# Kernel tuning notes

Measured on AMD Instinct MI355X. Metric: run time of the kernel, lower is better.

## Reference

```python
import jax, jax.numpy as jnp
import numpy as np

B, D, H, W = 2, 32, 192, 192
N_SIGMA = 3
K = 8  # max instance id; ids are 1..K, 0 = background
FG_W = 1.0
W_INST, W_VAR, W_SEED = 1.0, 10.0, 1.0


def _make_xyzm():
    # channel 0 = x (varies along W), 1 = y (along H), 2 = z (along D); pixel_{x,y,z}=1
    xm = jnp.broadcast_to(jnp.linspace(0.0, 1.0, W).reshape(1, 1, W), (D, H, W))
    ym = jnp.broadcast_to(jnp.linspace(0.0, 1.0, H).reshape(1, H, 1), (D, H, W))
    zm = jnp.broadcast_to(jnp.linspace(0.0, 1.0, D).reshape(D, 1, 1), (D, H, W))
    return jnp.stack([xm, ym, zm], 0)  # (3, D, H, W)


def setup_inputs() -> dict:
    key = jax.random.key(0)
    k1, k2, k3, k4 = jax.random.split(key, 4)
    prediction = jax.random.normal(k1, (B, 3 + N_SIGMA + 1, D, H, W), jnp.float32)
    instances = jax.random.randint(k2, (B, D, H, W), 0, K + 1, jnp.int32)
    labels = jax.random.randint(k3, (B, D, H, W), 0, 2, jnp.int32)
    center_images = jax.random.uniform(k4, (B, D, H, W)) < 5e-4  # sparse center flags
    return {"prediction": prediction, "xyzm": _make_xyzm(),
            "instances": instances, "labels": labels, "center_images": center_images}


def _lovasz_hinge_flat(logits, labels):
    # logits, labels: (N,) flat; labels in {0,1} float
    signs = 2.0 * labels - 1.0
    errors = 1.0 - logits * signs
    order = jnp.argsort(-errors)          # descending errors
    errors_s = errors[order]
    gt_s = labels[order]
    gts = gt_s.sum()
    inter = gts - jnp.cumsum(gt_s)
    union = gts + jnp.cumsum(1.0 - gt_s)
    jacc = 1.0 - inter / union
    grad = jnp.concatenate([jacc[:1], jacc[1:] - jacc[:-1]])
    return jnp.dot(jax.nn.relu(errors_s), jax.lax.stop_gradient(grad))


def _forward(prediction, xyzm, instances, labels, center_images):
    def per_batch(pred, inst, lab, cim):
        emb = jnp.tanh(pred[0:3]) + xyzm                      # (3,D,H,W)
        sigma = pred[3:3 + N_SIGMA]                           # (ns,D,H,W)
        seed = jax.nn.sigmoid(pred[3 + N_SIGMA])              # (D,H,W)
        ids = jnp.arange(1, K + 1)
        masks = (inst[None] == ids[:, None, None, None]).astype(pred.dtype)  # (K,D,H,W)
        counts = masks.sum(axis=(1, 2, 3))                    # (K,)
        valid = counts > 0
        safe = jnp.maximum(counts, 1.0)
        # center: single flagged center voxel if exactly one, else masked mean of coords
        mean_center = jnp.einsum('kdhw,cdhw->kc', masks, xyzm) / safe[:, None]
        cmask = masks * cim[None].astype(pred.dtype)
        cm_cnt = cmask.sum(axis=(1, 2, 3))
        cm_center = jnp.einsum('kdhw,cdhw->kc', cmask, xyzm)
        center = jnp.where((cm_cnt == 1.0)[:, None], cm_center, mean_center)  # (K,3)
        # sigma stats per instance; var term vs detached mean, expanded form
        m_sig = jnp.einsum('kdhw,cdhw->kc', masks, sigma)
        m_sig2 = jnp.einsum('kdhw,cdhw->kc', masks, sigma * sigma)
        s_mean = m_sig / safe[:, None]                        # (K,ns)
        s_sg = jax.lax.stop_gradient(s_mean)
        var_sum = m_sig2 - 2.0 * s_sg * m_sig + s_sg * s_sg * counts[:, None]
        var_k = var_sum.sum(1) / (N_SIGMA * safe)
        s_exp = jnp.exp(10.0 * s_mean)                        # (K,ns)
        # sum_c s_c*(emb_c-center_c)^2, expanded to avoid a (K,3,D,H,W) temp
        d2 = (jnp.einsum('kc,cdhw->kdhw', s_exp, emb * emb)
              - 2.0 * jnp.einsum('kc,cdhw->kdhw', s_exp * center, emb)
              + (s_exp * center * center).sum(1)[:, None, None, None])
        dist = jnp.exp(-d2)                                   # (K,D,H,W)
        inst_k = jax.vmap(_lovasz_hinge_flat)(
            (2.0 * dist - 1.0).reshape(K, -1), masks.reshape(K, -1))
        obj = jnp.maximum(valid.sum(), 1).astype(pred.dtype)
        instance_loss = jnp.where(valid, inst_k, 0.0).sum() / obj
        var_loss = jnp.where(valid, var_k, 0.0).sum() / obj
        bg = (lab == 0).astype(pred.dtype)
        seed_loss = (bg * seed * seed).sum()
        seed_loss = seed_loss + FG_W * (masks * (seed[None] - jax.lax.stop_gradient(dist)) ** 2).sum()
        seed_loss = seed_loss / (D * H * W)
        return W_INST * instance_loss + W_VAR * var_loss + W_SEED * seed_loss

    losses = jax.vmap(per_batch)(prediction, instances, labels, center_images)
    return losses.mean()


def reference(prediction, xyzm, instances, labels, center_images):
    return _forward(prediction, xyzm, instances, labels, center_images)
```

## Files before the change

### kernel.cpp

```cpp
#include <hip/hip_runtime.h>
#include <stdint.h>

typedef unsigned long long u64;
typedef unsigned int u32;

#define BN 2
#define DD 32
#define HH 192
#define WW 192
#define NV (DD*HH*WW)
#define KK 8
#define NSL 288
#define VPB 4096
#define NB 256
#define BOFF 1808
#define L2E 1.44269504f
#define SSLOT 11

__device__ __forceinline__ u64 fx(float v){ return (u64)(long long)llrintf(v*4294967296.0f); }
__device__ __forceinline__ float unfx(u64 v){ return (float)((double)(long long)v*(1.0/4294967296.0)); }
__device__ __forceinline__ float rcp_f(float x){ return __builtin_amdgcn_rcpf(x); }
__device__ __forceinline__ float exp2_f(float x){ return __builtin_amdgcn_exp2f(x); }
__device__ __forceinline__ float tanh_f(float x){ return 1.f - 2.f*rcp_f(1.f + exp2_f(x*(2.f*L2E))); }
__device__ __forceinline__ float sigm_f(float x){ return rcp_f(1.f + exp2_f(-x*L2E)); }
__device__ __forceinline__ float rfl(float x){ return __uint_as_float(__builtin_amdgcn_readfirstlane((int)__float_as_uint(x))); }

__global__ void k_detect(const u32* __restrict__ w, int nwords, u32* flags){
    u32 fF=0,fB=0,fO=0,f1=0;
    for (int i = blockIdx.x*blockDim.x + threadIdx.x; i < nwords; i += gridDim.x*blockDim.x){
        u32 x = w[i];
        if (x == 0x3F800000u) fF = 1;
        else if (x > 1u) fB = 1;
        else if (x == 1u){ f1 = 1; if (i & 1) fO = 1; }
    }
    if (fF) atomicOr(&flags[0], 1u);
    if (fB) atomicOr(&flags[1], 1u);
    if (fO) atomicOr(&flags[2], 1u);
    if (f1) atomicOr(&flags[3], 1u);
}

__global__ __launch_bounds__(512, 8) void k_stats(
        const float* __restrict__ pred,
        const int* __restrict__ inst,
        const void* __restrict__ cim, const u32* __restrict__ flags,
        u64* __restrict__ ssh, u64* __restrict__ bgsh){
    int sx = blockIdx.x, b = blockIdx.y;
    __shared__ u64 bins[8][4][25];
    __shared__ u64 cmb[8][KK][4];
    for (int i = threadIdx.x; i < 8*4*25; i += 512) ((u64*)bins)[i] = 0ull;
    for (int i = threadIdx.x; i < 8*KK*4; i += 512) ((u64*)cmb)[i] = 0ull;
    __syncthreads();
    int mode = flags[0] ? 2 : (flags[1] ? 1 : (flags[2] ? 0 : (flags[3] ? 3 : 0)));
    const float* pb = pred + (size_t)b*7*NV;
    const int* ib = inst + (size_t)b*NV;
    int wv = threadIdx.x >> 6, lp = threadIdx.x & 3;
    int g = sx*VPB + threadIdx.x*8;

    const float4* q0p = (const float4*)&pb[3*(size_t)NV + g];
    const float4* q1p = (const float4*)&pb[4*(size_t)NV + g];
    const float4* q2p = (const float4*)&pb[5*(size_t)NV + g];
    float4 sa0 = q0p[0], sb0 = q0p[1];
    float4 sa1 = q1p[0], sb1 = q1p[1];
    float4 sa2 = q2p[0], sb2 = q2p[1];
    const int4* qi = (const int4*)&ib[g];
    int4 i0 = qi[0], i1 = qi[1];
    int iy = g / WW;
    int ix = g - iy*WW;
    int iz = iy / HH; iy -= iz*HH;
    u64 fxm = fx(ix*(1.f/(WW-1)));
    u64 fdx = fx(1.f/(WW-1));
    u64 fym = fx(iy*(1.f/(HH-1)));
    u64 fzm = fx(iz*(1.f/(DD-1)));
    u32 cv8 = 0;
    size_t gi = (size_t)b*NV + g;
    if (mode == 0){
        int4 c0 = ((const int4*)&((const int*)cim)[gi])[0];
        int4 c1 = ((const int4*)&((const int*)cim)[gi])[1];
        cv8 = (c0.x?1u:0u)|(c0.y?2u:0u)|(c0.z?4u:0u)|(c0.w?8u:0u)
            | (c1.x?16u:0u)|(c1.y?32u:0u)|(c1.z?64u:0u)|(c1.w?128u:0u);
    } else if (mode == 1){
        u64 c = *(const u64*)&((const unsigned char*)cim)[gi];
        #pragma unroll
        for (int j = 0; j < 8; j++) if ((c >> (8*j)) & 0xFFull) cv8 |= 1u << j;
    } else if (mode == 2){
        float4 c0 = ((const float4*)&((const float*)cim)[gi])[0];
        float4 c1 = ((const float4*)&((const float*)cim)[gi])[1];
        cv8 = (c0.x!=0.f?1u:0u)|(c0.y!=0.f?2u:0u)|(c0.z!=0.f?4u:0u)|(c0.w!=0.f?8u:0u)
            | (c1.x!=0.f?16u:0u)|(c1.y!=0.f?32u:0u)|(c1.z!=0.f?64u:0u)|(c1.w!=0.f?128u:0u);
    } else {
        const int4* cc = (const int4*)&((const int*)cim)[2*gi];
        int4 c0 = cc[0], c1 = cc[1], c2 = cc[2], c3 = cc[3];
        cv8 = (c0.x?1u:0u)|(c0.z?2u:0u)|(c1.x?4u:0u)|(c1.z?8u:0u)
            | (c2.x?16u:0u)|(c2.z?32u:0u)|(c3.x?64u:0u)|(c3.z?128u:0u);
    }
    float s0a[8] = {sa0.x,sa0.y,sa0.z,sa0.w,sb0.x,sb0.y,sb0.z,sb0.w};
    float s1a[8] = {sa1.x,sa1.y,sa1.z,sa1.w,sb1.x,sb1.y,sb1.z,sb1.w};
    float s2a[8] = {sa2.x,sa2.y,sa2.z,sa2.w,sb2.x,sb2.y,sb2.z,sb2.w};
    int iva[8] = {i0.x,i0.y,i0.z,i0.w,i1.x,i1.y,i1.z,i1.w};
    #pragma unroll
    for (int j = 0; j < 8; j++){
        int iv = iva[j];
        if (iv >= 1 && iv <= KK){
            u64* bn = &bins[wv][lp][(iv-1)*3];
            u32 cv = (cv8 >> j) & 1u;
            u32 q0 = (u32)llrintf((s0a[j] + 16.f)*4096.f);
            u32 q1 = (u32)llrintf((s1a[j] + 16.f)*4096.f);
            u32 q2 = (u32)llrintf((s2a[j] + 16.f)*4096.f);
            float s2t = s0a[j]*s0a[j] + s1a[j]*s1a[j] + s2a[j]*s2a[j];
            u32 r = (u32)llrintf(fminf(s2t, 512.f)*2048.f);
            atomicAdd(&bn[0], (1ull << 44) | ((u64)(u32)(ix + j) << 24) | ((u64)(u32)iy << 4) | cv);
            atomicAdd(&bn[1], ((u64)q0 << 32) | q1);
            atomicAdd(&bn[2], ((u64)q2 << 32) | r);
            if (cv){
                u64* cb = &cmb[wv][iv-1][0];
                atomicAdd(&cb[0], fxm + (u64)j*fdx);
                atomicAdd(&cb[1], fym);
                atomicAdd(&cb[2], fzm);
            }
        }
    }
    __syncthreads();
    int t = threadIdx.x;
    u64* cell0 = &ssh[((size_t)((sx&3)*BN + b))*KK*SSLOT];
    if (t < KK){
        int k = t;
        u64 sA = 0ull, sB = 0ull, sC = 0ull;
        #pragma unroll
        for (int r2 = 0; r2 < 32; r2++){
            const u64* bn = &bins[r2>>2][r2&3][k*3];
            sA += bn[0]; sB += bn[1]; sC += bn[2];
        }
        u64 cnt = sA >> 44;
        if (cnt){
            u64 six = (sA >> 24) & 0xFFFFFull;
            u64 siy = (sA >> 4) & 0xFFFFFull;
            u64 cm  = sA & 0xFull;
            long long bias = (long long)(cnt * 65536ull);
            long long g0 = (long long)(sB >> 32) - bias;
            long long g1 = (long long)(sB & 0xFFFFFFFFull) - bias;
            long long g2 = (long long)(sC >> 32) - bias;
            u64 h = sC & 0xFFFFFFFFull;
            u64* cell = cell0 + (size_t)k*SSLOT;
            atomicAdd(&cell[0], (cnt << 32) | cm);
            atomicAdd(&cell[1], six);
            atomicAdd(&cell[2], siy);
            atomicAdd(&cell[3], cnt*(u64)iz);
            atomicAdd(&cell[4], (u64)g0);
            atomicAdd(&cell[5], (u64)g1);
            atomicAdd(&cell[6], (u64)g2);
            atomicAdd(&cell[7], h);
        }
    }
    if (t < KK*3){
        int k = t / 3, s = t - k*3;
        u64 acc = 0ull;
        #pragma unroll
        for (int w = 0; w < 8; w++) acc += cmb[w][k][s];
        if (acc) atomicAdd(&cell0[(size_t)k*SSLOT + 8 + s], acc);
    }
}

__global__ void k_derive(const u64* __restrict__ ssh, float* __restrict__ derived,
                         float* __restrict__ var_part){
    int t = threadIdx.x;
    __shared__ float s_val[16], s_vrk[16], s_obj[2];
    if (t < 16){
        int bb = t >> 3, kq = t & 7;
        u64 st[SSLOT];
        #pragma unroll
        for (int s = 0; s < SSLOT; s++){
            u64 a = 0ull;
            #pragma unroll
            for (int sh = 0; sh < 4; sh++)
                a += ssh[((size_t)(sh*BN + bb)*KK + kq)*SSLOT + s];
            st[s] = a;
        }
        float cnt = (float)(long long)(st[0] >> 32);
        float cmc = (float)(u32)st[0];
        float mx = (float)(long long)st[1] * (1.f/(WW-1));
        float my = (float)(long long)st[2] * (1.f/(HH-1));
        float mz = (float)(long long)st[3] * (1.f/(DD-1));
        float g0 = (float)((double)(long long)st[4] * (1.0/4096.0));
        float g1 = (float)((double)(long long)st[5] * (1.0/4096.0));
        float g2 = (float)((double)(long long)st[6] * (1.0/4096.0));
        float h  = (float)((double)(long long)st[7] * (1.0/2048.0));
        float cmx = unfx(st[8]), cmy = unfx(st[9]), cmz = unfx(st[10]);
        float valid = cnt > 0.f ? 1.f : 0.f;
        float safe = fmaxf(cnt, 1.f);
        float isafe = 1.f/safe;
        float c0 = (cmc == 1.f) ? cmx : mx*isafe;
        float c1 = (cmc == 1.f) ? cmy : my*isafe;
        float c2 = (cmc == 1.f) ? cmz : mz*isafe;
        float sm0 = g0*isafe, sm1 = g1*isafe, sm2 = g2*isafe;
        float vs = h - 2.f*(sm0*g0 + sm1*g1 + sm2*g2)
                 + (sm0*sm0 + sm1*sm1 + sm2*sm2)*cnt;
        s_vrk[t] = vs*isafe*(1.f/3.f);
        s_val[t] = valid;
        float* dd = &derived[(size_t)t*8];
        dd[0] = expf(10.f*sm0)*L2E; dd[1] = expf(10.f*sm1)*L2E; dd[2] = expf(10.f*sm2)*L2E;
        dd[3] = c0; dd[4] = c1; dd[5] = c2; dd[6] = cnt;
    }
    __syncthreads();
    if (t < 2){
        float obj = 0.f, vp = 0.f;
        #pragma unroll
        for (int kq = 0; kq < 8; kq++){
            obj += s_val[t*8 + kq];
            vp += s_val[t*8 + kq]*s_vrk[t*8 + kq];
        }
        obj = fmaxf(obj, 1.f);
        var_part[t] = vp / obj;
        s_obj[t] = obj;
    }
    __syncthreads();
    if (t < 16) derived[(size_t)t*8 + 7] = s_val[t]/s_obj[t >> 3];
}

__global__ __launch_bounds__(512, 4) void k_hist(
        const float* __restrict__ pred,
        const int* __restrict__ inst, const int* __restrict__ lab,
        const float* __restrict__ derived,
        u32* __restrict__ hs, u64* __restrict__ bgsh){
    __shared__ u32 lh[KK*2*NB];
    __shared__ u64 fgfx, bgfx;
    int sx = blockIdx.x, b = blockIdx.y;
    if (threadIdx.x == 0){ fgfx = 0ull; bgfx = 0ull; }
    for (int i = threadIdx.x; i < KK*2*NB; i += 512) lh[i] = 0u;
    float ax[KK], ay[KK], az[KK], cx[KK], cy[KK], cz[KK];
    const float* db = derived + (size_t)b*KK*8;
    #pragma unroll
    for (int k = 0; k < KK; k++){
        ax[k]=rfl(db[k*8+0]); ay[k]=rfl(db[k*8+1]); az[k]=rfl(db[k*8+2]);
        cx[k]=rfl(db[k*8+3]); cy[k]=rfl(db[k*8+4]); cz[k]=rfl(db[k*8+5]);
    }
    __syncthreads();
    const float* pb = pred + (size_t)b*7*NV;
    const int* ib = inst + (size_t)b*NV;
    const int* lb = lab + (size_t)b*NV;
    int g = sx*VPB + threadIdx.x*8;
    const float4* q0 = (const float4*)&pb[g];
    const float4* q1 = (const float4*)&pb[(size_t)NV + g];
    const float4* q2 = (const float4*)&pb[2*(size_t)NV + g];
    const float4* q6 = (const float4*)&pb[6*(size_t)NV + g];
    float4 a0 = q0[0], b0 = q0[1];
    float4 a1 = q1[0], b1 = q1[1];
    float4 a2 = q2[0], b2 = q2[1];
    float4 a6 = q6[0], b6 = q6[1];
    const int4* qi = (const int4*)&ib[g];
    int4 i0 = qi[0], i1 = qi[1];
    const int4* ql = (const int4*)&lb[g];
    int4 l0 = ql[0], l1 = ql[1];
    int iy = g / WW;
    int ix = g - iy*WW;
    int iz = iy / HH; iy -= iz*HH;
    float xm = ix*(1.f/(WW-1)), ym = iy*(1.f/(HH-1)), zm = iz*(1.f/(DD-1));
    float p0a[8] = {a0.x,a0.y,a0.z,a0.w,b0.x,b0.y,b0.z,b0.w};
    float p1a[8] = {a1.x,a1.y,a1.z,a1.w,b1.x,b1.y,b1.z,b1.w};
    float p2a[8] = {a2.x,a2.y,a2.z,a2.w,b2.x,b2.y,b2.z,b2.w};
    float p6a[8] = {a6.x,a6.y,a6.z,a6.w,b6.x,b6.y,b6.z,b6.w};
    int iva[8] = {i0.x,i0.y,i0.z,i0.w,i1.x,i1.y,i1.z,i1.w};
    int lba[8] = {l0.x,l0.y,l0.z,l0.w,l1.x,l1.y,l1.z,l1.w};
    float e0[8], e1[8], e2[8], sd[8];
    float bgacc = 0.f;
    #pragma unroll
    for (int j = 0; j < 8; j++){
        e0[j] = tanh_f(p0a[j]) + xm + j*(1.f/(WW-1));
        e1[j] = tanh_f(p1a[j]) + ym;
        e2[j] = tanh_f(p2a[j]) + zm;
        sd[j] = sigm_f(p6a[j]);
        if (lba[j] == 0) bgacc += sd[j]*sd[j];
    }
    float fgacc = 0.f;
    #pragma unroll
    for (int k = 0; k < KK; k++){
        #pragma unroll
        for (int j = 0; j < 8; j++){
            float d0 = e0[j] - cx[k], d1 = e1[j] - cy[k], dz = e2[j] - cz[k];
            float d2 = ax[k]*d0*d0;
            d2 = fmaf(ay[k]*d1, d1, d2);
            d2 = fmaf(az[k]*dz, dz, d2);
            float dist = exp2_f(-d2);
            if (iva[j] == k + 1){
                float e = fmaf(-2.f, dist, 2.f);
                int bu = (int)(__float_as_uint(e) >> 19) - BOFF;
                bu = bu < 0 ? 0 : (bu > NB-1 ? NB-1 : bu);
                atomicAdd(&lh[k*512 + bu], 1u);
                fgacc += (sd[j] - dist)*(sd[j] - dist);
            } else {
                int bu = (int)(__float_as_uint(dist) >> 19) - (BOFF - 16);
                bu = bu < 0 ? 0 : (bu > NB-1 ? NB-1 : bu);
                atomicAdd(&lh[k*512 + NB + bu], 1u);
            }
        }
    }
    #pragma unroll
    for (int off = 32; off > 0; off >>= 1){
        fgacc += __shfl_down(fgacc, off);
        bgacc += __shfl_down(bgacc, off);
    }
    if ((threadIdx.x & 63) == 0){
        if (fgacc != 0.f) atomicAdd(&fgfx, fx(fgacc));
        if (bgacc != 0.f) atomicAdd(&bgfx, fx(bgacc));
    }
    __syncthreads();
    if (threadIdx.x == 0){
        if (bgfx) atomicAdd(&bgsh[(size_t)b*8 + (sx&7)], bgfx);
        if (fgfx) atomicAdd(&bgsh[(size_t)(2+b)*8 + (sx&7)], fgfx);
    }
    u32* out = hs + ((size_t)b*NSL + sx)*(KK*NB);
    for (int i = threadIdx.x; i < KK*NB; i += 512){
        int k = i >> 8, bu = i & 255;
        out[i] = (lh[k*512 + bu] << 16) | lh[k*512 + NB + bu];
    }
}

__global__ __launch_bounds__(1024) void k_lovasz(
        const u32* __restrict__ hs, const float* __restrict__ derived,
        float* __restrict__ lov, const float* __restrict__ var_part,
        const u64* __restrict__ bgsh, u32* __restrict__ counter,
        float* __restrict__ out){
    int bk = blockIdx.x, b = bk >> 3, k = bk & 7;
    int t = threadIdx.x;
    float gts = derived[(size_t)bk*8 + 6];
    float lv = 0.f;
    __shared__ u64 part[4][NB];
    __shared__ u64 wsum[4];
    __shared__ float racc[NB];
    if (gts >= 0.5f){
        int bu = (NB - 1) - (t & 255);
        int sg = t >> 8;
        u32 np = 0, nn = 0;
        const u32* base = hs + (size_t)b*NSL*(KK*NB) + k*NB + bu;
        for (int s = sg; s < NSL; s += 4){
            u32 h = base[(size_t)s*(KK*NB)];
            np += h >> 16; nn += h & 0xFFFFu;
        }
        part[sg][t & 255] = ((u64)np << 32) | nn;
        __syncthreads();
        u64 pack = 0ull, inc = 0ull;
        if (t < NB){
            pack = part[0][t] + part[1][t] + part[2][t] + part[3][t];
            int lane = t & 63;
            inc = pack;
            #pragma unroll
            for (int off = 1; off < 64; off <<= 1){
                u64 n = __shfl_up(inc, off);
                if (lane >= off) inc += n;
            }
            if (lane == 63) wsum[t >> 6] = inc;
        }
        __syncthreads();
        if (t < 4){
            u64 x = wsum[t];
            #pragma unroll
            for (int off = 1; off < 4; off <<= 1){
                u64 n = __shfl_up(x, off);
                if (t >= off) x += n;
            }
            wsum[t] = x;
        }
        __syncthreads();
        float acc = 0.f;
        if (t < NB){
            int wid = t >> 6;
            u64 excl = inc - pack + (wid ? wsum[wid - 1] : 0ull);
            u32 np2 = (u32)(pack >> 32), nn2 = (u32)pack;
            if (np2 | nn2){
                int bu2 = (NB - 1) - t;
                float Pe = (float)(u32)(excl >> 32), Qe = (float)(u32)excl;
                float Pi = Pe + (float)np2, Qi = Qe + (float)nn2;
                float je = 1.f - (gts - Pe)/(gts + Qe);
                float ji = 1.f - (gts - Pi)/(gts + Qi);
                u32 bits = ((u32)(bu2 + BOFF) << 19) | (1u << 18);
                if (bits > 0x40000000u) bits = 0x40000000u;
                acc = __uint_as_float(bits) * (ji - je);
            }
            racc[t] = acc;
        }
        __syncthreads();
        for (int off = 128; off > 0; off >>= 1){
            if (t < off) racc[t] += racc[t + off];
            __syncthreads();
        }
        lv = derived[(size_t)bk*8 + 7] * racc[0];
    }
    if (t == 0){
        __hip_atomic_store(&lov[bk], lv, __ATOMIC_RELEASE, __HIP_MEMORY_SCOPE_AGENT);
        u32 ticket = __hip_atomic_fetch_add(counter, 1u, __ATOMIC_ACQ_REL, __HIP_MEMORY_SCOPE_AGENT);
        if (ticket == 15u){
            float tot = 0.f;
            for (int i = 0; i < 16; i++)
                tot += __hip_atomic_load(&lov[i], __ATOMIC_ACQUIRE, __HIP_MEMORY_SCOPE_AGENT);
            for (int b2 = 0; b2 < BN; b2++){
                float bg = 0.f, fg = 0.f;
                for (int sh = 0; sh < 8; sh++){
                    bg += unfx(bgsh[(size_t)b2*8 + sh]);
                    fg += unfx(bgsh[(size_t)(2+b2)*8 + sh]);
                }
                tot += 10.f*var_part[b2] + (bg + fg)*(1.f/(float)NV);
            }
            out[0] = tot * 0.5f;
        }
    }
}

extern "C" void kernel_launch(void* const* d_in, const int* in_sizes, int n_in,
                              void* d_out, int out_size, void* d_ws, size_t ws_size,
                              hipStream_t stream){
    const float* pred = (const float*)d_in[0];
    const int*   inst = (const int*)d_in[2];
    const int*   lab  = (const int*)d_in[3];
    const void*  cim  = d_in[4];

    char* ws = (char*)d_ws;
    size_t off = 0;
    u32* hs = (u32*)(ws + off);        off += (size_t)BN*NSL*KK*NB*4;
    size_t small0 = off;
    u64* ssh = (u64*)(ws + off);       off += (size_t)4*BN*KK*SSLOT*8;
    u64* bgsh = (u64*)(ws + off);      off += (size_t)4*8*8;
    float* derived = (float*)(ws + off); off += (size_t)BN*KK*8*4;
    float* lov = (float*)(ws + off);   off += 16*4;
    float* var_part = (float*)(ws + off); off += 2*4;
    u32* flags = (u32*)(ws + off);     off += 4*4;
    u32* counter = (u32*)(ws + off);   off += 4;

    (void)hipMemsetAsync(ws + small0, 0, off - small0, stream);
    k_detect<<<dim3(256), dim3(256), 0, stream>>>((const u32*)cim, BN*NV/4, flags);
    k_stats<<<dim3(NSL, BN), dim3(512), 0, stream>>>(pred, inst, cim, flags, ssh, bgsh);
    k_derive<<<1, 64, 0, stream>>>(ssh, derived, var_part);
    k_hist<<<dim3(NSL, BN), dim3(512), 0, stream>>>(pred, inst, lab, derived, hs, bgsh);
    k_lovasz<<<16, 1024, 0, stream>>>(hs, derived, lov, var_part, bgsh, counter, (float*)d_out);
}
```

Measured before the change: 78.05 us.

## Fold memset and derive kernel into neighbouring kernels to cut launches

```diff
diff --git a/kernel.cpp b/kernel.cpp
--- a/kernel.cpp
+++ b/kernel.cpp
@@ -16,6 +16,7 @@
 #define BOFF 1808
 #define L2E 1.44269504f
 #define SSLOT 11
+#define NFRONT 16
 
 __device__ __forceinline__ u64 fx(float v){ return (u64)(long long)llrintf(v*4294967296.0f); }
 __device__ __forceinline__ float unfx(u64 v){ return (float)((double)(long long)v*(1.0/4294967296.0)); }
@@ -25,32 +26,74 @@
 __device__ __forceinline__ float sigm_f(float x){ return rcp_f(1.f + exp2_f(-x*L2E)); }
 __device__ __forceinline__ float rfl(float x){ return __uint_as_float(__builtin_amdgcn_readfirstlane((int)__float_as_uint(x))); }
 
-__global__ void k_detect(const u32* __restrict__ w, int nwords, u32* flags){
-    u32 fF=0,fB=0,fO=0,f1=0;
-    for (int i = blockIdx.x*blockDim.x + threadIdx.x; i < nwords; i += gridDim.x*blockDim.x){
+struct Cell { float cnt, cmc, mx, my, mz, g0, g1, g2, h, cmx, cmy, cmz; };
+__device__ __forceinline__ Cell load_cell(const u64* __restrict__ ssh, int bb, int kq){
+    u64 st[SSLOT];
+    #pragma unroll
+    for (int s = 0; s < SSLOT; s++){
+        u64 a = 0ull;
+        #pragma unroll
+        for (int sh = 0; sh < 4; sh++)
+            a += ssh[((size_t)(sh*BN + bb)*KK + kq)*SSLOT + s];
+        st[s] = a;
+    }
+    Cell c;
+    c.cnt = (float)(long long)(st[0] >> 32);
+    c.cmc = (float)(u32)st[0];
+    c.mx = (float)(long long)st[1] * (1.f/(WW-1));
+    c.my = (float)(long long)st[2] * (1.f/(HH-1));
+    c.mz = (float)(long long)st[3] * (1.f/(DD-1));
+    c.g0 = (float)((double)(long long)st[4] * (1.0/4096.0));
+    c.g1 = (float)((double)(long long)st[5] * (1.0/4096.0));
+    c.g2 = (float)((double)(long long)st[6] * (1.0/4096.0));
+    c.h  = (float)((double)(long long)st[7] * (1.0/2048.0));
+    c.cmx = unfx(st[8]); c.cmy = unfx(st[9]); c.cmz = unfx(st[10]);
+    return c;
+}
+
+__global__ __launch_bounds__(1024) void k_front(
+        const u32* __restrict__ w, u32* __restrict__ fpart,
+        u64* __restrict__ zero_base, int nzero_u64, u32* __restrict__ counter){
+    int bid = blockIdx.x;
+    if (bid == 0){
+        for (int i = threadIdx.x; i < nzero_u64; i += 1024) zero_base[i] = 0ull;
+        if (threadIdx.x == 0) *counter = 0u;
+    }
+    __shared__ u32 lfl;
+    if (threadIdx.x == 0) lfl = 0u;
+    __syncthreads();
+    const int chunk = (BN*NV/4)/NFRONT;
+    u32 f = 0;
+    for (int i = bid*chunk + threadIdx.x; i < (bid+1)*chunk; i += 1024){
         u32 x = w[i];
-        if (x == 0x3F800000u) fF = 1;
-        else if (x > 1u) fB = 1;
-        else if (x == 1u){ f1 = 1; if (i & 1) fO = 1; }
-    }
-    if (fF) atomicOr(&flags[0], 1u);
-    if (fB) atomicOr(&flags[1], 1u);
-    if (fO) atomicOr(&flags[2], 1u);
-    if (f1) atomicOr(&flags[3], 1u);
+        if (x == 0x3F800000u) f |= 1u;
+        else if (x > 1u) f |= 2u;
+        else if (x == 1u){ f |= 8u; if (i & 1) f |= 4u; }
+    }
+    if (f) atomicOr(&lfl, f);
+    __syncthreads();
+    if (threadIdx.x == 0) fpart[bid] = lfl;
 }
 
 __global__ __launch_bounds__(512, 8) void k_stats(
         const float* __restrict__ pred,
         const int* __restrict__ inst,
-        const void* __restrict__ cim, const u32* __restrict__ flags,
-        u64* __restrict__ ssh, u64* __restrict__ bgsh){
+        const void* __restrict__ cim, const u32* __restrict__ fpart,
+        u64* __restrict__ ssh){
     int sx = blockIdx.x, b = blockIdx.y;
     __shared__ u64 bins[8][4][25];
     __shared__ u64 cmb[8][KK][4];
+    __shared__ int smode;
     for (int i = threadIdx.x; i < 8*4*25; i += 512) ((u64*)bins)[i] = 0ull;
     for (int i = threadIdx.x; i < 8*KK*4; i += 512) ((u64*)cmb)[i] = 0ull;
-    __syncthreads();
-    int mode = flags[0] ? 2 : (flags[1] ? 1 : (flags[2] ? 0 : (flags[3] ? 3 : 0)));
+    if (threadIdx.x == 0){
+        u32 fl = 0;
+        #pragma unroll
+        for (int i = 0; i < NFRONT; i++) fl |= fpart[i];
+        smode = (fl & 1u) ? 2 : ((fl & 2u) ? 1 : ((fl & 4u) ? 0 : ((fl & 8u) ? 3 : 0)));
+    }
+    __syncthreads();
+    int mode = smode;
     const float* pb = pred + (size_t)b*7*NV;
     const int* ib = inst + (size_t)b*NV;
     int wv = threadIdx.x >> 6, lp = threadIdx.x & 3;
@@ -160,80 +203,36 @@
     }
 }
 
-__global__ void k_derive(const u64* __restrict__ ssh, float* __restrict__ derived,
-                         float* __restrict__ var_part){
-    int t = threadIdx.x;
-    __shared__ float s_val[16], s_vrk[16], s_obj[2];
-    if (t < 16){
-        int bb = t >> 3, kq = t & 7;
-        u64 st[SSLOT];
-        #pragma unroll
-        for (int s = 0; s < SSLOT; s++){
-            u64 a = 0ull;
-            #pragma unroll
-            for (int sh = 0; sh < 4; sh++)
-                a += ssh[((size_t)(sh*BN + bb)*KK + kq)*SSLOT + s];
-            st[s] = a;
-        }
-        float cnt = (float)(long long)(st[0] >> 32);
-        float cmc = (float)(u32)st[0];
-        float mx = (float)(long long)st[1] * (1.f/(WW-1));
-        float my = (float)(long long)st[2] * (1.f/(HH-1));
-        float mz = (float)(long long)st[3] * (1.f/(DD-1));
-        float g0 = (float)((double)(long long)st[4] * (1.0/4096.0));
-        float g1 = (float)((double)(long long)st[5] * (1.0/4096.0));
-        float g2 = (float)((double)(long long)st[6] * (1.0/4096.0));
-        float h  = (float)((double)(long long)st[7] * (1.0/2048.0));
-        float cmx = unfx(st[8]), cmy = unfx(st[9]), cmz = unfx(st[10]);
-        float valid = cnt > 0.f ? 1.f : 0.f;
-        float safe = fmaxf(cnt, 1.f);
-        float isafe = 1.f/safe;
-        float c0 = (cmc == 1.f) ? cmx : mx*isafe;
-        float c1 = (cmc == 1.f) ? cmy : my*isafe;
-        float c2 = (cmc == 1.f) ? cmz : mz*isafe;
-        float sm0 = g0*isafe, sm1 = g1*isafe, sm2 = g2*isafe;
-        float vs = h - 2.f*(sm0*g0 + sm1*g1 + sm2*g2)
-                 + (sm0*sm0 + sm1*sm1 + sm2*sm2)*cnt;
-        s_vrk[t] = vs*isafe*(1.f/3.f);
-        s_val[t] = valid;
-        float* dd = &derived[(size_t)t*8];
-        dd[0] = expf(10.f*sm0)*L2E; dd[1] = expf(10.f*sm1)*L2E; dd[2] = expf(10.f*sm2)*L2E;
-        dd[3] = c0; dd[4] = c1; dd[5] = c2; dd[6] = cnt;
-    }
-    __syncthreads();
-    if (t < 2){
-        float obj = 0.f, vp = 0.f;
-        #pragma unroll
-        for (int kq = 0; kq < 8; kq++){
-            obj += s_val[t*8 + kq];
-            vp += s_val[t*8 + kq]*s_vrk[t*8 + kq];
-        }
-        obj = fmaxf(obj, 1.f);
-        var_part[t] = vp / obj;
-        s_obj[t] = obj;
-    }
-    __syncthreads();
-    if (t < 16) derived[(size_t)t*8 + 7] = s_val[t]/s_obj[t >> 3];
-}
-
 __global__ __launch_bounds__(512, 4) void k_hist(
-        const float* __restrict__ pred,
+        const u64* __restrict__ ssh, const float* __restrict__ pred,
         const int* __restrict__ inst, const int* __restrict__ lab,
-        const float* __restrict__ derived,
         u32* __restrict__ hs, u64* __restrict__ bgsh){
     __shared__ u32 lh[KK*2*NB];
     __shared__ u64 fgfx, bgfx;
+    __shared__ float dv[KK*6];
     int sx = blockIdx.x, b = blockIdx.y;
     if (threadIdx.x == 0){ fgfx = 0ull; bgfx = 0ull; }
     for (int i = threadIdx.x; i < KK*2*NB; i += 512) lh[i] = 0u;
+    if (threadIdx.x < KK){
+        int kq = threadIdx.x;
+        Cell c = load_cell(ssh, b, kq);
+        float safe = fmaxf(c.cnt, 1.f);
+        float isafe = 1.f/safe;
+        float c0 = (c.cmc == 1.f) ? c.cmx : c.mx*isafe;
+        float c1 = (c.cmc == 1.f) ? c.cmy : c.my*isafe;
+        float c2 = (c.cmc == 1.f) ? c.cmz : c.mz*isafe;
+        dv[kq*6+0] = expf(10.f*c.g0*isafe)*L2E;
+        dv[kq*6+1] = expf(10.f*c.g1*isafe)*L2E;
+        dv[kq*6+2] = expf(10.f*c.g2*isafe)*L2E;
+        dv[kq*6+3] = c0; dv[kq*6+4] = c1; dv[kq*6+5] = c2;
+    }
+    __syncthreads();
     float ax[KK], ay[KK], az[KK], cx[KK], cy[KK], cz[KK];
-    const float* db = derived + (size_t)b*KK*8;
     #pragma unroll
     for (int k = 0; k < KK; k++){
-        ax[k]=rfl(db[k*8+0]); ay[k]=rfl(db[k*8+1]); az[k]=rfl(db[k*8+2]);
-        cx[k]=rfl(db[k*8+3]); cy[k]=rfl(db[k*8+4]); cz[k]=rfl(db[k*8+5]);
-    }
-    __syncthreads();
+        ax[k]=rfl(dv[k*6+0]); ay[k]=rfl(dv[k*6+1]); az[k]=rfl(dv[k*6+2]);
+        cx[k]=rfl(dv[k*6+3]); cy[k]=rfl(dv[k*6+4]); cz[k]=rfl(dv[k*6+5]);
+    }
     const float* pb = pred + (size_t)b*7*NV;
     const int* ib = inst + (size_t)b*NV;
     const int* lb = lab + (size_t)b*NV;
@@ -315,13 +314,28 @@
 }
 
 __global__ __launch_bounds__(1024) void k_lovasz(
-        const u32* __restrict__ hs, const float* __restrict__ derived,
-        float* __restrict__ lov, const float* __restrict__ var_part,
-        const u64* __restrict__ bgsh, u32* __restrict__ counter,
-        float* __restrict__ out){
+        const u32* __restrict__ hs, const u64* __restrict__ ssh,
+        float* __restrict__ lov, const u64* __restrict__ bgsh,
+        u32* __restrict__ counter, float* __restrict__ out){
     int bk = blockIdx.x, b = bk >> 3, k = bk & 7;
     int t = threadIdx.x;
-    float gts = derived[(size_t)bk*8 + 6];
+    __shared__ float s_cnt[16], s_vrk[16], s_val[16];
+    if (t < 16){
+        Cell c = load_cell(ssh, t >> 3, t & 7);
+        float safe = fmaxf(c.cnt, 1.f);
+        float isafe = 1.f/safe;
+        float sm0 = c.g0*isafe, sm1 = c.g1*isafe, sm2 = c.g2*isafe;
+        float vs = c.h - 2.f*(sm0*c.g0 + sm1*c.g1 + sm2*c.g2)
+                 + (sm0*sm0 + sm1*sm1 + sm2*sm2)*c.cnt;
+        s_vrk[t] = vs*isafe*(1.f/3.f);
+        s_val[t] = c.cnt > 0.f ? 1.f : 0.f;
+        s_cnt[t] = c.cnt;
+    }
+    __syncthreads();
+    float gts = s_cnt[bk];
+    float obj = fmaxf(s_val[b*8+0]+s_val[b*8+1]+s_val[b*8+2]+s_val[b*8+3]
+                     +s_val[b*8+4]+s_val[b*8+5]+s_val[b*8+6]+s_val[b*8+7], 1.f);
+    float coef = s_val[bk]/obj;
     float lv = 0.f;
     __shared__ u64 part[4][NB];
     __shared__ u64 wsum[4];
@@ -382,7 +396,7 @@
             if (t < off) racc[t] += racc[t + off];
             __syncthreads();
         }
-        lv = derived[(size_t)bk*8 + 7] * racc[0];
+        lv = coef * racc[0];
     }
     if (t == 0){
         __hip_atomic_store(&lov[bk], lv, __ATOMIC_RELEASE, __HIP_MEMORY_SCOPE_AGENT);
@@ -392,12 +406,16 @@
             for (int i = 0; i < 16; i++)
                 tot += __hip_atomic_load(&lov[i], __ATOMIC_ACQUIRE, __HIP_MEMORY_SCOPE_AGENT);
             for (int b2 = 0; b2 < BN; b2++){
+                float objb = fmaxf(s_val[b2*8+0]+s_val[b2*8+1]+s_val[b2*8+2]+s_val[b2*8+3]
+                                  +s_val[b2*8+4]+s_val[b2*8+5]+s_val[b2*8+6]+s_val[b2*8+7], 1.f);
+                float vp = 0.f;
+                for (int kq = 0; kq < 8; kq++) vp += s_val[b2*8+kq]*s_vrk[b2*8+kq];
                 float bg = 0.f, fg = 0.f;
                 for (int sh = 0; sh < 8; sh++){
                     bg += unfx(bgsh[(size_t)b2*8 + sh]);
                     fg += unfx(bgsh[(size_t)(2+b2)*8 + sh]);
                 }
-                tot += 10.f*var_part[b2] + (bg + fg)*(1.f/(float)NV);
+                tot += 10.f*vp/objb + (bg + fg)*(1.f/(float)NV);
             }
             out[0] = tot * 0.5f;
         }
@@ -415,19 +433,17 @@
     char* ws = (char*)d_ws;
     size_t off = 0;
     u32* hs = (u32*)(ws + off);        off += (size_t)BN*NSL*KK*NB*4;
-    size_t small0 = off;
+    size_t zero0 = off;
     u64* ssh = (u64*)(ws + off);       off += (size_t)4*BN*KK*SSLOT*8;
     u64* bgsh = (u64*)(ws + off);      off += (size_t)4*8*8;
-    float* derived = (float*)(ws + off); off += (size_t)BN*KK*8*4;
+    size_t zero_u64 = (off - zero0)/8;
     float* lov = (float*)(ws + off);   off += 16*4;
-    float* var_part = (float*)(ws + off); off += 2*4;
-    u32* flags = (u32*)(ws + off);     off += 4*4;
     u32* counter = (u32*)(ws + off);   off += 4;
-
-    (void)hipMemsetAsync(ws + small0, 0, off - small0, stream);
-    k_detect<<<dim3(256), dim3(256), 0, stream>>>((const u32*)cim, BN*NV/4, flags);
-    k_stats<<<dim3(NSL, BN), dim3(512), 0, stream>>>(pred, inst, cim, flags, ssh, bgsh);
-    k_derive<<<1, 64, 0, stream>>>(ssh, derived, var_part);
-    k_hist<<<dim3(NSL, BN), dim3(512), 0, stream>>>(pred, inst, lab, derived, hs, bgsh);
-    k_lovasz<<<16, 1024, 0, stream>>>(hs, derived, lov, var_part, bgsh, counter, (float*)d_out);
-}
+    u32* fpart = (u32*)(ws + off);     off += NFRONT*4;
+
+    k_front<<<dim3(NFRONT), dim3(1024), 0, stream>>>((const u32*)cim, fpart,
+                                                     (u64*)(ws + zero0), (int)zero_u64, counter);
+    k_stats<<<dim3(NSL, BN), dim3(512), 0, stream>>>(pred, inst, cim, fpart, ssh);
+    k_hist<<<dim3(NSL, BN), dim3(512), 0, stream>>>(ssh, pred, inst, lab, hs, bgsh);
+    k_lovasz<<<16, 1024, 0, stream>>>(hs, ssh, lov, bgsh, counter, (float*)d_out);
+}
```

New measurement: 70.66 us. -9.5%, faster.
